# Kernel optimization log

Measured on AMD Instinct MI355X. Metric: run time of the kernel, lower is better.

Reference implementation:

```python
import jax, jax.numpy as jnp
import numpy as np
from jax import lax

B, S, I, H = 256, 512, 128, 256  # batch, seq_len, input_size, hidden_size
SCALE = 0.05


def _lstm_layer(x, Wih, Whh, bih, bhh):
    """Run one LSTMCell layer over time. x: [B, S, D]. Returns (y [B,S,H], h, c)."""
    b, _, _ = x.shape
    h0 = jnp.zeros((b, Whh.shape[1]), dtype=x.dtype)
    c0 = jnp.zeros((b, Whh.shape[1]), dtype=x.dtype)
    WihT, WhhT = Wih.T, Whh.T
    bias = bih + bhh

    def step(carry, xt):
        h, c = carry
        gates = xt @ WihT + h @ WhhT + bias  # [B, 4H]
        i, f, g, o = jnp.split(gates, 4, axis=-1)  # torch gate order: i, f, g, o
        i = jax.nn.sigmoid(i)
        f = jax.nn.sigmoid(f)
        g = jnp.tanh(g)
        o = jax.nn.sigmoid(o)
        c = f * c + i * g
        h = o * jnp.tanh(c)
        return (h, c), h

    (h, c), ys = lax.scan(step, (h0, c0), jnp.swapaxes(x, 0, 1))  # scan over time
    return jnp.swapaxes(ys, 0, 1), h, c


def setup_inputs() -> dict:
    key = jax.random.key(0)
    ks = jax.random.split(key, 9)
    x = jax.random.normal(ks[0], (B, S, I), dtype=jnp.float32)
    d = {"x": x}
    d["W_ih0"] = jax.random.normal(ks[1], (4 * H, I), dtype=jnp.float32) * SCALE
    d["W_hh0"] = jax.random.normal(ks[2], (4 * H, H), dtype=jnp.float32) * SCALE
    d["b_ih0"] = jax.random.normal(ks[3], (4 * H,), dtype=jnp.float32) * SCALE
    d["b_hh0"] = jax.random.normal(ks[4], (4 * H,), dtype=jnp.float32) * SCALE
    d["W_ih1"] = jax.random.normal(ks[5], (4 * H, H), dtype=jnp.float32) * SCALE
    d["W_hh1"] = jax.random.normal(ks[6], (4 * H, H), dtype=jnp.float32) * SCALE
    d["b_ih1"] = jax.random.normal(ks[7], (4 * H,), dtype=jnp.float32) * SCALE
    d["b_hh1"] = jax.random.normal(ks[8], (4 * H,), dtype=jnp.float32) * SCALE
    return d


def reference(x, W_ih0, W_hh0, b_ih0, b_hh0, W_ih1, W_hh1, b_ih1, b_hh1):
    # Layer 1 over raw input, layer 2 over layer-1 outputs (eval mode: no dropout).
    y, h, c = _lstm_layer(x, W_ih0, W_hh0, b_ih0, b_hh0)
    y, h, c = _lstm_layer(y, W_ih1, W_hh1, b_ih1, b_hh1)
    return y, (h[None, :, :], c[None, :, :])
```

## Files before the change

kernel.cpp:

```cpp
#include <hip/hip_runtime.h>
#include <hip/hip_bf16.h>

#define BB 256
#define SS 512
#define II 128
#define HH 256

typedef __attribute__((ext_vector_type(8))) __bf16 bf16x8;
typedef __attribute__((ext_vector_type(4))) float f32x4;

__device__ __forceinline__ unsigned short f2bf(float f) {
    unsigned u = __float_as_uint(f);
    unsigned r = u + 0x7fffu + ((u >> 16) & 1u);
    return (unsigned short)(r >> 16);
}

__global__ void pack_w_kernel(const float* __restrict__ Wih,
                              const float* __restrict__ Whh,
                              unsigned short* __restrict__ wp,
                              int Kin, int nkc) {
    int idx = blockIdx.x * blockDim.x + threadIdx.x;
    int total = 64 * nkc * 64;
    if (idx >= total) return;
    int nblk = idx / (nkc * 64);
    int rem  = idx % (nkc * 64);
    int kc = rem >> 6;
    int L  = rem & 63;
    int p  = nblk * 16 + (L & 15);
    int s  = p >> 6;
    int q6 = p & 63;
    int nw = q6 >> 5;
    int nb = (q6 >> 4) & 1;
    int c  = q6 & 15;
    int gam = nb * 2 + (c >> 3);
    int u   = s * 16 + nw * 8 + (c & 7);
    int srow = gam * HH + u;
    int k0 = kc * 32 + (L >> 4) * 8;
    unsigned short* dst = wp + (size_t)idx * 8;
    for (int j = 0; j < 8; ++j) {
        int k = k0 + j;
        float v = (k < Kin) ? Wih[(size_t)srow * Kin + k]
                            : Whh[(size_t)srow * HH + (k - Kin)];
        dst[j] = f2bf(v);
    }
}

__global__ void pack_bias_kernel(const float* bi0, const float* bh0,
                                 const float* bi1, const float* bh1,
                                 float* __restrict__ biasP) {
    int p = blockIdx.x * blockDim.x + threadIdx.x;
    if (p >= 2048) return;
    int layer = p >> 10;
    int pp = p & 1023;
    int s  = pp >> 6;
    int q6 = pp & 63;
    int nw = q6 >> 5;
    int nb = (q6 >> 4) & 1;
    int c  = q6 & 15;
    int gam = nb * 2 + (c >> 3);
    int u   = s * 16 + nw * 8 + (c & 7);
    int r = gam * HH + u;
    biasP[p] = layer ? (bi1[r] + bh1[r]) : (bi0[r] + bh0[r]);
}

__device__ __forceinline__ bool wait_slots(unsigned int* p, unsigned tgt) {
    long it = 0;
    for (;;) {
        unsigned v = __hip_atomic_load(p, __ATOMIC_RELAXED, __HIP_MEMORY_SCOPE_AGENT);
        if (__all((int)(v >= tgt))) return true;
        __builtin_amdgcn_s_sleep(1);
        if (++it > 2000000l) return false;
    }
}

template <int LAYER>
__device__ __forceinline__ void run_layer(
    int bid, const float* __restrict__ x,
    const unsigned short* __restrict__ wp,
    const float* __restrict__ biasP,
    unsigned short* __restrict__ Y0,
    unsigned short* __restrict__ Y1,
    unsigned int* __restrict__ slots,
    float* __restrict__ out,
    unsigned short* As, int* abort_flag) {

    constexpr int KIN = LAYER ? HH : II;
    constexpr int KC  = KIN + HH;
    constexpr int NKC = KC >> 5;
    constexpr int KCP = KC + 8;

    const int g = (bid >> 4) & 7;
    const int s = bid & 15;
    const int tid = threadIdx.x;
    const int L = tid & 63;
    const int w = tid >> 6;
    const int mw = w & 1;
    const int nwv = w >> 1;
    const int c = L & 15;
    const int b0 = g * 32;

    const unsigned short* wB0 = wp + ((size_t)((s * 4 + nwv * 2 + 0) * NKC) * 64 + L) * 8;
    const unsigned short* wB1 = wp + ((size_t)((s * 4 + nwv * 2 + 1) * NKC) * 64 + L) * 8;
    bf16x8 w0r[NKC], w1r[NKC];
#pragma unroll
    for (int kc = 0; kc < NKC; ++kc) {
        w0r[kc] = *(const bf16x8*)(wB0 + (size_t)kc * 512);
        w1r[kc] = *(const bf16x8*)(wB1 + (size_t)kc * 512);
    }
    const float bq0 = biasP[LAYER * 1024 + s * 64 + nwv * 32 + c];
    const float bq1 = biasP[LAYER * 1024 + s * 64 + nwv * 32 + 16 + c];

    float cst[4] = {0.f, 0.f, 0.f, 0.f};

    float* outY  = out;
    float* outHn = out + (size_t)BB * SS * HH;
    float* outCn = outHn + (size_t)BB * HH;
    unsigned long long* Y0l = (unsigned long long*)Y0;
    unsigned long long* Y1l = (unsigned long long*)Y1;
    unsigned int* Y0u = (unsigned int*)Y0;
    unsigned int* Y1u = (unsigned int*)Y1;

    unsigned int* slotsG0 = slots + (size_t)((0 * 8 + g) * 16) * 32;
    unsigned int* slotsG1 = slots + (size_t)((1 * 8 + g) * 16) * 32;
    unsigned int* myslot  = (LAYER ? slotsG1 : slotsG0) + s * 32;
    unsigned int* pollp;
    unsigned tgt_off;
    if (LAYER == 0) {
        pollp = slotsG0 + (L & 15) * 32;
        tgt_off = 0u;
    } else {
        int idx = L & 31;
        pollp = (idx < 16) ? (slotsG0 + idx * 32)
                           : (slotsG1 + (idx - 16) * 32);
        tgt_off = (idx < 16) ? 1u : 0u;
    }

    const int row8 = tid >> 3;
    const int c8   = tid & 7;
    const int rowb = tid >> 5;
    const int cc   = tid & 31;

    for (int t = 0; t < SS; ++t) {
        unsigned long long yv[8];
        float4 xv[4];

        if (LAYER == 0) {
#pragma unroll
            for (int k = 0; k < 4; ++k) {
                int row = rowb + 8 * k;
                xv[k] = *(const float4*)(x + ((size_t)(b0 + row) * SS + t) * II + cc * 4);
            }
            if (w == 0 && t > 0) {
                if (!wait_slots(pollp, (unsigned)t) && L == 0) *abort_flag = 1;
            }
            __syncthreads();
            if (*abort_flag) return;
        } else {
            if (w == 0) {
                unsigned tgt = (unsigned)t + tgt_off;
                if (!wait_slots(pollp, tgt) && L == 0) *abort_flag = 1;
            }
            __syncthreads();
            if (*abort_flag) return;
            {
                unsigned long long* sp = Y0l + ((size_t)t * BB + b0 + row8) * 64;
#pragma unroll
                for (int j = 0; j < 8; ++j)
                    yv[j] = __hip_atomic_load(sp + c8 + 8 * j, __ATOMIC_RELAXED,
                                              __HIP_MEMORY_SCOPE_AGENT);
            }
        }

        unsigned long long hv[8];
        if (t > 0) {
            unsigned long long* sp = (LAYER == 0)
                ? Y0l + ((size_t)(t - 1) * BB + b0 + row8) * 64
                : Y1l + ((size_t)((t - 1) & 3) * BB + b0 + row8) * 64;
#pragma unroll
            for (int j = 0; j < 8; ++j)
                hv[j] = __hip_atomic_load(sp + c8 + 8 * j, __ATOMIC_RELAXED,
                                          __HIP_MEMORY_SCOPE_AGENT);
        } else {
#pragma unroll
            for (int j = 0; j < 8; ++j) hv[j] = 0ull;
        }

        if (LAYER == 0) {
#pragma unroll
            for (int k = 0; k < 4; ++k) {
                int row = rowb + 8 * k;
                ushort4 pk;
                pk.x = f2bf(xv[k].x); pk.y = f2bf(xv[k].y);
                pk.z = f2bf(xv[k].z); pk.w = f2bf(xv[k].w);
                *(ushort4*)&As[row * KCP + cc * 4] = pk;
            }
        } else {
#pragma unroll
            for (int j = 0; j < 8; ++j)
                *(unsigned long long*)&As[row8 * KCP + (c8 + 8 * j) * 4] = yv[j];
        }
#pragma unroll
        for (int j = 0; j < 8; ++j)
            *(unsigned long long*)&As[row8 * KCP + KIN + (c8 + 8 * j) * 4] = hv[j];
        __syncthreads();

        f32x4 acc0 = {0.f, 0.f, 0.f, 0.f};
        f32x4 acc1 = {0.f, 0.f, 0.f, 0.f};
        const unsigned short* aBase = &As[(mw * 16 + c) * KCP + (L >> 4) * 8];
#pragma unroll
        for (int kc = 0; kc < NKC; ++kc) {
            bf16x8 a = *(const bf16x8*)(aBase + kc * 32);
            acc0 = __builtin_amdgcn_mfma_f32_16x16x32_bf16(a, w0r[kc], acc0, 0, 0, 0);
            acc1 = __builtin_amdgcn_mfma_f32_16x16x32_bf16(a, w1r[kc], acc1, 0, 0, 0);
        }

#pragma unroll
        for (int r = 0; r < 4; ++r) {
            float x0 = acc0[r] + bq0;
            float x1 = acc1[r] + bq1;
            float y0v = __shfl_xor(x0, 8, 64);
            float y1v = __shfl_xor(x1, 8, 64);
            bool lo = (L & 8) == 0;
            float iv = lo ? x0 : y0v;
            float fv = lo ? y0v : x0;
            float gv = lo ? x1 : y1v;
            float ov = lo ? y1v : x1;
            iv = 1.f / (1.f + __expf(-iv));
            fv = 1.f / (1.f + __expf(-fv));
            ov = 1.f / (1.f + __expf(-ov));
            gv = 1.f - 2.f / (1.f + __expf(2.f * gv));
            float cn = fv * cst[r] + iv * gv;
            cst[r] = cn;
            float tc = 1.f - 2.f / (1.f + __expf(2.f * cn));
            float hn = ov * tc;

            int brow = b0 + mw * 16 + ((L >> 4) << 2) + r;
            int hu = s * 16 + nwv * 8 + (L & 7);
            unsigned hb = (unsigned)f2bf(hn);
            unsigned pb = (unsigned)__shfl_xor((int)hb, 1, 64);
            unsigned packed = hb | (pb << 16);
            if (lo && (L & 1) == 0) {
                size_t di = (((size_t)(LAYER == 0 ? t * BB : (size_t)(t & 3) * BB)
                              + brow) * HH + hu) >> 1;
                unsigned old = __hip_atomic_exchange(
                    (LAYER == 0 ? Y0u : Y1u) + di, packed,
                    __ATOMIC_RELAXED, __HIP_MEMORY_SCOPE_AGENT);
                asm volatile("" :: "v"(old));
            }
            if (LAYER == 1 && lo) {
                outY[((size_t)brow * SS + t) * HH + hu] = hn;
                if (t == SS - 1) {
                    outHn[brow * HH + hu] = hn;
                    outCn[brow * HH + hu] = cn;
                }
            }
        }

        __syncthreads();
        if (tid == 0) {
            unsigned old = __hip_atomic_exchange(myslot, (unsigned)(t + 1),
                                                 __ATOMIC_RELAXED,
                                                 __HIP_MEMORY_SCOPE_AGENT);
            asm volatile("" :: "v"(old));
        }
    }
}

__global__ __launch_bounds__(256, 1) void lstm_main(
    const float* __restrict__ x,
    const unsigned short* __restrict__ wp0,
    const unsigned short* __restrict__ wp1,
    const float* __restrict__ biasP,
    unsigned short* __restrict__ Y0,
    unsigned short* __restrict__ Y1,
    unsigned int* __restrict__ slots,
    float* __restrict__ out) {

    __shared__ unsigned short As[32 * 520];
    __shared__ int abort_flag;
    if (threadIdx.x == 0) abort_flag = 0;

    int bid = blockIdx.x;
    if (bid < 128)
        run_layer<0>(bid, x, wp0, biasP, Y0, Y1, slots, out, As, &abort_flag);
    else
        run_layer<1>(bid, x, wp1, biasP, Y0, Y1, slots, out, As, &abort_flag);
}

extern "C" void kernel_launch(void* const* d_in, const int* in_sizes, int n_in,
                              void* d_out, int out_size, void* d_ws, size_t ws_size,
                              hipStream_t stream) {
    const float* x    = (const float*)d_in[0];
    const float* Wih0 = (const float*)d_in[1];
    const float* Whh0 = (const float*)d_in[2];
    const float* bih0 = (const float*)d_in[3];
    const float* bhh0 = (const float*)d_in[4];
    const float* Wih1 = (const float*)d_in[5];
    const float* Whh1 = (const float*)d_in[6];
    const float* bih1 = (const float*)d_in[7];
    const float* bhh1 = (const float*)d_in[8];

    char* ws = (char*)d_ws;
    size_t o = 0;
    unsigned short* wp0 = (unsigned short*)(ws + o); o += (size_t)64 * 12 * 512 * 2;
    unsigned short* wp1 = (unsigned short*)(ws + o); o += (size_t)64 * 16 * 512 * 2;
    float* biasP = (float*)(ws + o);                 o += 2048 * 4;
    unsigned short* Y0 = (unsigned short*)(ws + o);  o += (size_t)SS * BB * HH * 2;
    unsigned short* Y1 = (unsigned short*)(ws + o);  o += (size_t)4 * BB * HH * 2;
    unsigned int* slots = (unsigned int*)(ws + o);   o += (size_t)2 * 8 * 16 * 32 * 4;

    hipMemsetAsync(slots, 0, (size_t)2 * 8 * 16 * 32 * 4, stream);
    pack_w_kernel<<<192, 256, 0, stream>>>(Wih0, Whh0, wp0, II, 12);
    pack_w_kernel<<<256, 256, 0, stream>>>(Wih1, Whh1, wp1, HH, 16);
    pack_bias_kernel<<<8, 256, 0, stream>>>(bih0, bhh0, bih1, bhh1, biasP);
    lstm_main<<<256, 256, 0, stream>>>(x, wp0, wp1, biasP, Y0, Y1, slots, (float*)d_out);
}
```

Measured before the change: 2.868 ms.

## Replace layer-0 slot counters with sentinel-based data polling on Y0

Layer 0 blocks, and layer 1's reads of layer-0 output, no longer wait on per-block step counters. Y0 is pre-filled with 0xFF sentinels and consumers spin on the data itself until no 32-bit word equals the sentinel. This removes the counter round-trip and the end-of-step barrier plus counter publish in layer 0, shortening the recurrent critical path. The cost is a 64 MB memset each call and repeated polling of data lines. It also relies on no valid packed bf16 pair ever equalling 0xFFFFFFFF; an extra barrier after the MFMA protects the shared-memory tile.

```diff
diff --git a/kernel.cpp b/kernel.cpp
--- a/kernel.cpp
+++ b/kernel.cpp
@@ -73,6 +73,26 @@
     }
 }
 
+__device__ __forceinline__ void poll_gather(unsigned long long* sp, int c8,
+                                            unsigned long long* v,
+                                            int* abort_flag) {
+    long it = 0;
+    for (;;) {
+#pragma unroll
+        for (int j = 0; j < 8; ++j)
+            v[j] = __hip_atomic_load(sp + c8 + 8 * j, __ATOMIC_RELAXED,
+                                     __HIP_MEMORY_SCOPE_AGENT);
+        unsigned ok = 1u;
+#pragma unroll
+        for (int j = 0; j < 8; ++j)
+            ok &= ((unsigned)v[j] != 0xFFFFFFFFu) &
+                  ((unsigned)(v[j] >> 32) != 0xFFFFFFFFu);
+        if (__all((int)ok)) return;
+        __builtin_amdgcn_s_sleep(1);
+        if (++it > 1000000l) { *abort_flag = 1; return; }
+    }
+}
+
 template <int LAYER>
 __device__ __forceinline__ void run_layer(
     int bid, const float* __restrict__ x,
@@ -120,20 +140,8 @@
     unsigned int* Y0u = (unsigned int*)Y0;
     unsigned int* Y1u = (unsigned int*)Y1;
 
-    unsigned int* slotsG0 = slots + (size_t)((0 * 8 + g) * 16) * 32;
     unsigned int* slotsG1 = slots + (size_t)((1 * 8 + g) * 16) * 32;
-    unsigned int* myslot  = (LAYER ? slotsG1 : slotsG0) + s * 32;
-    unsigned int* pollp;
-    unsigned tgt_off;
-    if (LAYER == 0) {
-        pollp = slotsG0 + (L & 15) * 32;
-        tgt_off = 0u;
-    } else {
-        int idx = L & 31;
-        pollp = (idx < 16) ? (slotsG0 + idx * 32)
-                           : (slotsG1 + (idx - 16) * 32);
-        tgt_off = (idx < 16) ? 1u : 0u;
-    }
+    unsigned int* myslot  = slotsG1 + s * 32;
 
     const int row8 = tid >> 3;
     const int c8   = tid & 7;
@@ -142,6 +150,7 @@
 
     for (int t = 0; t < SS; ++t) {
         unsigned long long yv[8];
+        unsigned long long hv[8];
         float4 xv[4];
 
         if (LAYER == 0) {
@@ -150,42 +159,13 @@
                 int row = rowb + 8 * k;
                 xv[k] = *(const float4*)(x + ((size_t)(b0 + row) * SS + t) * II + cc * 4);
             }
-            if (w == 0 && t > 0) {
-                if (!wait_slots(pollp, (unsigned)t) && L == 0) *abort_flag = 1;
-            }
-            __syncthreads();
-            if (*abort_flag) return;
-        } else {
-            if (w == 0) {
-                unsigned tgt = (unsigned)t + tgt_off;
-                if (!wait_slots(pollp, tgt) && L == 0) *abort_flag = 1;
-            }
-            __syncthreads();
-            if (*abort_flag) return;
-            {
-                unsigned long long* sp = Y0l + ((size_t)t * BB + b0 + row8) * 64;
-#pragma unroll
-                for (int j = 0; j < 8; ++j)
-                    yv[j] = __hip_atomic_load(sp + c8 + 8 * j, __ATOMIC_RELAXED,
-                                              __HIP_MEMORY_SCOPE_AGENT);
-            }
-        }
-
-        unsigned long long hv[8];
-        if (t > 0) {
-            unsigned long long* sp = (LAYER == 0)
-                ? Y0l + ((size_t)(t - 1) * BB + b0 + row8) * 64
-                : Y1l + ((size_t)((t - 1) & 3) * BB + b0 + row8) * 64;
-#pragma unroll
-            for (int j = 0; j < 8; ++j)
-                hv[j] = __hip_atomic_load(sp + c8 + 8 * j, __ATOMIC_RELAXED,
-                                          __HIP_MEMORY_SCOPE_AGENT);
-        } else {
-#pragma unroll
-            for (int j = 0; j < 8; ++j) hv[j] = 0ull;
-        }
-
-        if (LAYER == 0) {
+            if (t > 0) {
+                poll_gather(Y0l + ((size_t)(t - 1) * BB + b0 + row8) * 64,
+                            c8, hv, abort_flag);
+            } else {
+#pragma unroll
+                for (int j = 0; j < 8; ++j) hv[j] = 0ull;
+            }
 #pragma unroll
             for (int k = 0; k < 4; ++k) {
                 int row = rowb + 8 * k;
@@ -194,15 +174,38 @@
                 pk.z = f2bf(xv[k].z); pk.w = f2bf(xv[k].w);
                 *(ushort4*)&As[row * KCP + cc * 4] = pk;
             }
+#pragma unroll
+            for (int j = 0; j < 8; ++j)
+                *(unsigned long long*)&As[row8 * KCP + KIN + (c8 + 8 * j) * 4] = hv[j];
+            __syncthreads();
+            if (*abort_flag) return;
         } else {
+            poll_gather(Y0l + ((size_t)t * BB + b0 + row8) * 64,
+                        c8, yv, abort_flag);
+            if (w == 0 && t > 0) {
+                if (!wait_slots(slotsG1 + (L & 15) * 32, (unsigned)t))
+                    *abort_flag = 1;
+            }
+            __syncthreads();
+            if (*abort_flag) return;
+            if (t > 0) {
+                unsigned long long* sp = Y1l + ((size_t)((t - 1) & 3) * BB + b0 + row8) * 64;
+#pragma unroll
+                for (int j = 0; j < 8; ++j)
+                    hv[j] = __hip_atomic_load(sp + c8 + 8 * j, __ATOMIC_RELAXED,
+                                              __HIP_MEMORY_SCOPE_AGENT);
+            } else {
+#pragma unroll
+                for (int j = 0; j < 8; ++j) hv[j] = 0ull;
+            }
 #pragma unroll
             for (int j = 0; j < 8; ++j)
                 *(unsigned long long*)&As[row8 * KCP + (c8 + 8 * j) * 4] = yv[j];
+#pragma unroll
+            for (int j = 0; j < 8; ++j)
+                *(unsigned long long*)&As[row8 * KCP + KIN + (c8 + 8 * j) * 4] = hv[j];
+            __syncthreads();
         }
-#pragma unroll
-        for (int j = 0; j < 8; ++j)
-            *(unsigned long long*)&As[row8 * KCP + KIN + (c8 + 8 * j) * 4] = hv[j];
-        __syncthreads();
 
         f32x4 acc0 = {0.f, 0.f, 0.f, 0.f};
         f32x4 acc1 = {0.f, 0.f, 0.f, 0.f};
@@ -213,6 +216,7 @@
             acc0 = __builtin_amdgcn_mfma_f32_16x16x32_bf16(a, w0r[kc], acc0, 0, 0, 0);
             acc1 = __builtin_amdgcn_mfma_f32_16x16x32_bf16(a, w1r[kc], acc1, 0, 0, 0);
         }
+        __syncthreads();
 
 #pragma unroll
         for (int r = 0; r < 4; ++r) {
@@ -240,12 +244,18 @@
             unsigned pb = (unsigned)__shfl_xor((int)hb, 1, 64);
             unsigned packed = hb | (pb << 16);
             if (lo && (L & 1) == 0) {
-                size_t di = (((size_t)(LAYER == 0 ? t * BB : (size_t)(t & 3) * BB)
-                              + brow) * HH + hu) >> 1;
-                unsigned old = __hip_atomic_exchange(
-                    (LAYER == 0 ? Y0u : Y1u) + di, packed,
-                    __ATOMIC_RELAXED, __HIP_MEMORY_SCOPE_AGENT);
-                asm volatile("" :: "v"(old));
+                if (LAYER == 0) {
+                    size_t di = (((size_t)t * BB + brow) * HH + hu) >> 1;
+                    (void)__hip_atomic_exchange(Y0u + di, packed,
+                                                __ATOMIC_RELAXED,
+                                                __HIP_MEMORY_SCOPE_AGENT);
+                } else {
+                    size_t di = (((size_t)(t & 3) * BB + brow) * HH + hu) >> 1;
+                    unsigned old = __hip_atomic_exchange(Y1u + di, packed,
+                                                         __ATOMIC_RELAXED,
+                                                         __HIP_MEMORY_SCOPE_AGENT);
+                    asm volatile("" :: "v"(old));
+                }
             }
             if (LAYER == 1 && lo) {
                 outY[((size_t)brow * SS + t) * HH + hu] = hn;
@@ -256,12 +266,14 @@
             }
         }
 
-        __syncthreads();
-        if (tid == 0) {
-            unsigned old = __hip_atomic_exchange(myslot, (unsigned)(t + 1),
-                                                 __ATOMIC_RELAXED,
-                                                 __HIP_MEMORY_SCOPE_AGENT);
-            asm volatile("" :: "v"(old));
+        if (LAYER == 1) {
+            __syncthreads();
+            if (tid == 0) {
+                unsigned old = __hip_atomic_exchange(myslot, (unsigned)(t + 1),
+                                                     __ATOMIC_RELAXED,
+                                                     __HIP_MEMORY_SCOPE_AGENT);
+                asm volatile("" :: "v"(old));
+            }
         }
     }
 }
@@ -279,6 +291,7 @@
     __shared__ unsigned short As[32 * 520];
     __shared__ int abort_flag;
     if (threadIdx.x == 0) abort_flag = 0;
+    __syncthreads();
 
     int bid = blockIdx.x;
     if (bid < 128)
@@ -309,6 +322,7 @@
     unsigned short* Y1 = (unsigned short*)(ws + o);  o += (size_t)4 * BB * HH * 2;
     unsigned int* slots = (unsigned int*)(ws + o);   o += (size_t)2 * 8 * 16 * 32 * 4;
 
+    hipMemsetAsync(Y0, 0xFF, (size_t)SS * BB * HH * 2, stream);
     hipMemsetAsync(slots, 0, (size_t)2 * 8 * 16 * 32 * 4, stream);
     pack_w_kernel<<<192, 256, 0, stream>>>(Wih0, Whh0, wp0, II, 12);
     pack_w_kernel<<<256, 256, 0, stream>>>(Wih1, Whh1, wp1, HH, 16);
```

After: 2.934 ms. 2.3% more time.
